# Optimization experiments

Hardware: AMD Instinct MI355X
Metric: run time of the kernel (lower is better)

## Reference

```python
import jax, jax.numpy as jnp
import numpy as np

N_NODES = 100000
N_EDGES = 1250000
D_FEAT = 64


def setup_inputs() -> dict:
    key = jax.random.key(0)
    k1, k2 = jax.random.split(key)
    x = jax.random.normal(k1, (N_NODES, D_FEAT), dtype=jnp.float32)
    edge_index = jax.random.randint(k2, (2, N_EDGES), 0, N_NODES, dtype=jnp.int64)
    return {"t": 0, "x": x, "edge_index": edge_index}


def reference(t, x, edge_index):
    # LGConv(normalize=False): out[i] = sum_{(j->i) in E} x[j]
    # adj_t SpMM expressed as gather + segment-sum scatter.
    src = edge_index[0]  # source/neighbor nodes
    dst = edge_index[1]  # destination nodes
    msgs = x[src]  # [E, D] gather
    out = jax.ops.segment_sum(msgs, dst, num_segments=N_NODES)  # [N, D]
    return out
```

## Files before the change

kernel.cpp:

```cpp
#include <hip/hip_runtime.h>

#define N_NODES 100000
#define N_EDGES 1250000
#define D_FEAT 64

#define NB_SHIFT 7
#define NODES_PER_B 128
#define N_BUCKETS ((N_NODES + NODES_PER_B - 1) / NODES_PER_B)
#define TROW (N_BUCKETS + 1)
#define NB_PAD 1024
#define MAX_BUCKET_EDGES 2048
#define SRC_BITS 17
#define SRC_MASK ((1u << SRC_BITS) - 1u)

#define CH 8192
#define NCH ((N_EDGES + CH - 1) / CH)

__global__ __launch_bounds__(256) void lgconv_scatter(
    const float* __restrict__ x, const int* __restrict__ src,
    const int* __restrict__ dst, float* __restrict__ out) {
    int tid  = blockIdx.x * blockDim.x + threadIdx.x;
    int edge = tid >> 4;
    int f4   = (tid & 15) << 2;
    if (edge >= N_EDGES) return;
    int s = src[edge], d = dst[edge];
    const float4 v = *reinterpret_cast<const float4*>(x + (size_t)s * D_FEAT + f4);
    float* o = out + (size_t)d * D_FEAT + f4;
    unsafeAtomicAdd(o + 0, v.x); unsafeAtomicAdd(o + 1, v.y);
    unsafeAtomicAdd(o + 2, v.z); unsafeAtomicAdd(o + 3, v.w);
}

__device__ __forceinline__ unsigned short f2bf(float f) {
    unsigned int u = __float_as_uint(f);
    return (unsigned short)((u + 0x7FFFu + ((u >> 16) & 1u)) >> 16);
}
__device__ __forceinline__ float bflo(unsigned int p) {
    return __uint_as_float(p << 16);
}
__device__ __forceinline__ float bfhi(unsigned int p) {
    return __uint_as_float(p & 0xFFFF0000u);
}

template <bool CONV>
__global__ __launch_bounds__(1024) void k1_sort(
    const float* __restrict__ x, unsigned short* __restrict__ xb,
    const int* __restrict__ src, const int* __restrict__ dst,
    unsigned int* __restrict__ bins, int* __restrict__ table) {
    __shared__ int hist[NB_PAD];
    __shared__ int scanBase[NB_PAD];
    __shared__ int cur[NB_PAD];
    __shared__ int scanTmp[1024];
    __shared__ unsigned int stage[CH];
    const int t    = threadIdx.x;
    const int c    = blockIdx.x;
    const int base = c * CH;
    const int cnt  = min(CH, N_EDGES - base);

    if (CONV) {
        const int F4 = N_NODES * D_FEAT / 4;
        for (int i = c * 1024 + t; i < F4; i += NCH * 1024) {
            float4 v = reinterpret_cast<const float4*>(x)[i];
            ushort4 o;
            o.x = f2bf(v.x); o.y = f2bf(v.y); o.z = f2bf(v.z); o.w = f2bf(v.w);
            reinterpret_cast<ushort4*>(xb)[i] = o;
        }
    }

    hist[t] = 0; cur[t] = 0;
    __syncthreads();
    for (int i = t; i < cnt; i += 1024)
        atomicAdd(&hist[dst[base + i] >> NB_SHIFT], 1);
    __syncthreads();
    int v = hist[t];
    scanTmp[t] = v;
    __syncthreads();
    for (int off = 1; off < 1024; off <<= 1) {
        int u = (t >= off) ? scanTmp[t - off] : 0;
        __syncthreads();
        scanTmp[t] += u;
        __syncthreads();
    }
    scanBase[t] = scanTmp[t] - v;
    __syncthreads();
    if (t < TROW) table[c * TROW + t] = scanBase[t];
    for (int i = t; i < cnt; i += 1024) {
        int d = dst[base + i], s = src[base + i];
        int b = d >> NB_SHIFT;
        unsigned int packed = ((unsigned int)(d & (NODES_PER_B - 1)) << SRC_BITS)
                            | (unsigned int)s;
        int pos = scanBase[b] + atomicAdd(&cur[b], 1);
        stage[pos] = packed;
    }
    __syncthreads();
    for (int i = t; i < cnt; i += 1024) bins[base + i] = stage[i];
}

template <bool BF>
__global__ __launch_bounds__(512) void k2_accum(
    const float* __restrict__ x, const unsigned short* __restrict__ xb,
    const unsigned int* __restrict__ bins, const int* __restrict__ table,
    float* __restrict__ out) {
    __shared__ int            startA[512];
    __shared__ unsigned short lenA[512];
    __shared__ int            destB[512];
    __shared__ int            scanTmp[512];
    __shared__ unsigned int   raw[MAX_BUCKET_EDGES];
    __shared__ unsigned int   srcs[MAX_BUCKET_EDGES];
    __shared__ int cntArr[NODES_PER_B];
    __shared__ int nodeOff[NODES_PER_B + 1];
    __shared__ int curN[NODES_PER_B];
    __shared__ int s2[NODES_PER_B];
    const int t = threadIdx.x;
    const int b = blockIdx.x;

    int st = 0, len = 0;
    if (t < NCH) {
        st  = table[t * TROW + b];
        len = table[t * TROW + b + 1] - st;
    }
    startA[t] = st;
    lenA[t]   = (unsigned short)len;
    scanTmp[t] = len;
    __syncthreads();
    for (int off = 1; off < 512; off <<= 1) {
        int u = (t >= off) ? scanTmp[t - off] : 0;
        __syncthreads();
        scanTmp[t] += u;
        __syncthreads();
    }
    destB[t] = scanTmp[t] - len;
    int cntTot = scanTmp[511];
    if (cntTot > MAX_BUCKET_EDGES) cntTot = MAX_BUCKET_EDGES;
    if (t < NODES_PER_B) cntArr[t] = 0;
    __syncthreads();

    {
        const int cj = t >> 4;
        const int jj = t & 15;
        for (int c0 = 0; c0 < NCH; c0 += 32) {
            int c = c0 + cj;
            if (c < NCH) {
                int l = lenA[c], s0 = startA[c], db = destB[c];
                const unsigned int* p = bins + (size_t)c * CH + s0;
                if (jj < l) raw[db + jj] = p[jj];
                if (jj == 15)
                    for (int q = 16; q < l; ++q) raw[db + q] = p[q];
            }
        }
    }
    __syncthreads();

    for (int i = t; i < cntTot; i += 512)
        atomicAdd(&cntArr[raw[i] >> SRC_BITS], 1);
    __syncthreads();
    int v = (t < NODES_PER_B) ? cntArr[t] : 0;
    if (t < NODES_PER_B) s2[t] = v;
    __syncthreads();
    for (int off = 1; off < NODES_PER_B; off <<= 1) {
        int u = (t < NODES_PER_B && t >= off) ? s2[t - off] : 0;
        __syncthreads();
        if (t < NODES_PER_B) s2[t] += u;
        __syncthreads();
    }
    if (t < NODES_PER_B) { nodeOff[t] = s2[t] - v; curN[t] = s2[t] - v; }
    if (t == 0) nodeOff[NODES_PER_B] = cntTot;
    __syncthreads();
    for (int i = t; i < cntTot; i += 512) {
        unsigned int p = raw[i];
        int pos = atomicAdd(&curN[p >> SRC_BITS], 1);
        srcs[pos] = p & SRC_MASK;
    }
    __syncthreads();

    if (BF) {
        const int wave = t >> 6;
        const int lane = t & 63;
        const int slot = lane >> 3;
        const int f0   = (lane & 7) << 3;
        for (int local = wave; local < NODES_PER_B; local += 8) {
            int beg = nodeOff[local], end = nodeOff[local + 1];
            float a0=0,a1=0,a2=0,a3=0,a4=0,a5=0,a6=0,a7=0;
            for (int k = beg + slot; k < end; k += 8) {
                const uint4 u = *reinterpret_cast<const uint4*>(
                    xb + (size_t)srcs[k] * D_FEAT + f0);
                a0 += bflo(u.x); a1 += bfhi(u.x);
                a2 += bflo(u.y); a3 += bfhi(u.y);
                a4 += bflo(u.z); a5 += bfhi(u.z);
                a6 += bflo(u.w); a7 += bfhi(u.w);
            }
            #pragma unroll
            for (int m = 8; m < 64; m <<= 1) {
                a0 += __shfl_xor(a0, m, 64); a1 += __shfl_xor(a1, m, 64);
                a2 += __shfl_xor(a2, m, 64); a3 += __shfl_xor(a3, m, 64);
                a4 += __shfl_xor(a4, m, 64); a5 += __shfl_xor(a5, m, 64);
                a6 += __shfl_xor(a6, m, 64); a7 += __shfl_xor(a7, m, 64);
            }
            int node = b * NODES_PER_B + local;
            if (slot == 0 && node < N_NODES) {
                float* op = out + (size_t)node * D_FEAT + f0;
                *reinterpret_cast<float4*>(op)     = make_float4(a0, a1, a2, a3);
                *reinterpret_cast<float4*>(op + 4) = make_float4(a4, a5, a6, a7);
            }
        }
    } else {
        int lane4 = (t & 15) << 2;
        for (int g = 0; g < NODES_PER_B / 32; ++g) {
            int local = g * 32 + (t >> 4);
            int node  = b * NODES_PER_B + local;
            int beg = nodeOff[local], end = nodeOff[local + 1];
            float4 acc = make_float4(0.f, 0.f, 0.f, 0.f);
            int k = beg;
            for (; k + 1 < end; k += 2) {
                unsigned int i0 = srcs[k], i1 = srcs[k + 1];
                const float4 a = *reinterpret_cast<const float4*>(x + (size_t)i0 * D_FEAT + lane4);
                const float4 c = *reinterpret_cast<const float4*>(x + (size_t)i1 * D_FEAT + lane4);
                acc.x += a.x + c.x; acc.y += a.y + c.y;
                acc.z += a.z + c.z; acc.w += a.w + c.w;
            }
            if (k < end) {
                unsigned int i0 = srcs[k];
                const float4 a = *reinterpret_cast<const float4*>(x + (size_t)i0 * D_FEAT + lane4);
                acc.x += a.x; acc.y += a.y; acc.z += a.z; acc.w += a.w;
            }
            if (node < N_NODES)
                *reinterpret_cast<float4*>(out + (size_t)node * D_FEAT + lane4) = acc;
        }
    }
}

extern "C" void kernel_launch(void* const* d_in, const int* in_sizes, int n_in,
                              void* d_out, int out_size, void* d_ws, size_t ws_size,
                              hipStream_t stream) {
    const float* x   = (const float*)d_in[1];
    const int*   ei  = (const int*)d_in[2];
    const int*   src = ei;
    const int*   dst = ei + N_EDGES;
    float*       out = (float*)d_out;

    const size_t tabBytes = (size_t)NCH * TROW * sizeof(int);
    const size_t binBytes = (size_t)N_EDGES * sizeof(unsigned int);
    const size_t xbOff    = (binBytes + tabBytes + 15) & ~(size_t)15;
    const size_t needA    = xbOff + (size_t)N_NODES * D_FEAT * sizeof(unsigned short);
    const size_t needB    = binBytes + tabBytes;

    if (ws_size >= needA) {
        unsigned int*   bins  = (unsigned int*)d_ws;
        int*            table = (int*)((char*)d_ws + binBytes);
        unsigned short* xb    = (unsigned short*)((char*)d_ws + xbOff);
        k1_sort<true><<<NCH, 1024, 0, stream>>>(x, xb, src, dst, bins, table);
        k2_accum<true><<<N_BUCKETS, 512, 0, stream>>>(x, xb, bins, table, out);
    } else if (ws_size >= needB) {
        unsigned int* bins  = (unsigned int*)d_ws;
        int*          table = (int*)((char*)d_ws + binBytes);
        k1_sort<false><<<NCH, 1024, 0, stream>>>(x, nullptr, src, dst, bins, table);
        k2_accum<false><<<N_BUCKETS, 512, 0, stream>>>(x, nullptr, bins, table, out);
    } else {
        hipMemsetAsync(out, 0, (size_t)out_size * sizeof(float), stream);
        const int total = N_EDGES * 16;
        lgconv_scatter<<<(total + 255) / 256, 256, 0, stream>>>(x, src, dst, out);
    }
}
```

Baseline: 142.9 us.

## Assign one node per 8 lanes in bf16 gather path, drop shuffle reduction

```diff
diff --git a/kernel.cpp b/kernel.cpp
--- a/kernel.cpp
+++ b/kernel.cpp
@@ -173,14 +173,32 @@
     __syncthreads();
 
     if (BF) {
-        const int wave = t >> 6;
-        const int lane = t & 63;
-        const int slot = lane >> 3;
-        const int f0   = (lane & 7) << 3;
-        for (int local = wave; local < NODES_PER_B; local += 8) {
+        int f0 = (t & 7) << 3;
+        for (int g = 0; g < NODES_PER_B / 64; ++g) {
+            int local = g * 64 + (t >> 3);
+            int node  = b * NODES_PER_B + local;
             int beg = nodeOff[local], end = nodeOff[local + 1];
             float a0=0,a1=0,a2=0,a3=0,a4=0,a5=0,a6=0,a7=0;
-            for (int k = beg + slot; k < end; k += 8) {
+            int k = beg;
+            for (; k + 3 < end; k += 4) {
+                const uint4 u0 = *reinterpret_cast<const uint4*>(
+                    xb + (size_t)srcs[k] * D_FEAT + f0);
+                const uint4 u1 = *reinterpret_cast<const uint4*>(
+                    xb + (size_t)srcs[k + 1] * D_FEAT + f0);
+                const uint4 u2 = *reinterpret_cast<const uint4*>(
+                    xb + (size_t)srcs[k + 2] * D_FEAT + f0);
+                const uint4 u3 = *reinterpret_cast<const uint4*>(
+                    xb + (size_t)srcs[k + 3] * D_FEAT + f0);
+                a0 += bflo(u0.x) + bflo(u1.x) + bflo(u2.x) + bflo(u3.x);
+                a1 += bfhi(u0.x) + bfhi(u1.x) + bfhi(u2.x) + bfhi(u3.x);
+                a2 += bflo(u0.y) + bflo(u1.y) + bflo(u2.y) + bflo(u3.y);
+                a3 += bfhi(u0.y) + bfhi(u1.y) + bfhi(u2.y) + bfhi(u3.y);
+                a4 += bflo(u0.z) + bflo(u1.z) + bflo(u2.z) + bflo(u3.z);
+                a5 += bfhi(u0.z) + bfhi(u1.z) + bfhi(u2.z) + bfhi(u3.z);
+                a6 += bflo(u0.w) + bflo(u1.w) + bflo(u2.w) + bflo(u3.w);
+                a7 += bfhi(u0.w) + bfhi(u1.w) + bfhi(u2.w) + bfhi(u3.w);
+            }
+            for (; k < end; ++k) {
                 const uint4 u = *reinterpret_cast<const uint4*>(
                     xb + (size_t)srcs[k] * D_FEAT + f0);
                 a0 += bflo(u.x); a1 += bfhi(u.x);
@@ -188,15 +206,7 @@
                 a4 += bflo(u.z); a5 += bfhi(u.z);
                 a6 += bflo(u.w); a7 += bfhi(u.w);
             }
-            #pragma unroll
-            for (int m = 8; m < 64; m <<= 1) {
-                a0 += __shfl_xor(a0, m, 64); a1 += __shfl_xor(a1, m, 64);
-                a2 += __shfl_xor(a2, m, 64); a3 += __shfl_xor(a3, m, 64);
-                a4 += __shfl_xor(a4, m, 64); a5 += __shfl_xor(a5, m, 64);
-                a6 += __shfl_xor(a6, m, 64); a7 += __shfl_xor(a7, m, 64);
-            }
-            int node = b * NODES_PER_B + local;
-            if (slot == 0 && node < N_NODES) {
+            if (node < N_NODES) {
                 float* op = out + (size_t)node * D_FEAT + f0;
                 *reinterpret_cast<float4*>(op)     = make_float4(a0, a1, a2, a3);
                 *reinterpret_cast<float4*>(op + 4) = make_float4(a4, a5, a6, a7);
```

Measured after the change: 136.8 us. -4.2%, faster.
